# Optimization experiments

Hardware: AMD Instinct MI355X
Metric: run time of the kernel (lower is better)

## Reference

```python
import jax, jax.numpy as jnp
import numpy as np

B, L, D, HD = 8, 4096, 1024, 16
H = D // HD


def setup_inputs() -> dict:
    key = jax.random.key(0)
    ks = jax.random.split(key, 16)
    s = 0.02
    return {
        "x": jax.random.normal(ks[0], (B, L, D), dtype=jnp.float32),
        "gamma": jnp.ones((D,), jnp.float32),
        "beta": jnp.zeros((D,), jnp.float32),
        "qw": jax.random.normal(ks[1], (D, D), jnp.float32) * s,
        "qb": jnp.zeros((D,), jnp.float32),
        "kw": jax.random.normal(ks[2], (D, D), jnp.float32) * s,
        "kb": jnp.zeros((D,), jnp.float32),
        "vw": jax.random.normal(ks[3], (D, D), jnp.float32) * s,
        "vb": jnp.zeros((D,), jnp.float32),
        "ow": jax.random.normal(ks[4], (D, D), jnp.float32) * s,
        "ob": jnp.zeros((D,), jnp.float32),
        "iw": jax.random.normal(ks[5], (H, D), jnp.float32) * s,
        "ib": jnp.zeros((H,), jnp.float32),
        "fw": jax.random.normal(ks[6], (H, D), jnp.float32) * s,
        "fb": jnp.zeros((H,), jnp.float32),
    }


def _layernorm(x, gamma, beta, eps=1e-5):
    mu = jnp.mean(x, axis=-1, keepdims=True)
    var = jnp.mean(jnp.square(x - mu), axis=-1, keepdims=True)
    return (x - mu) * jax.lax.rsqrt(var + eps) * gamma + beta


def _forward(x, gamma, beta, qw, qb, kw, kb, vw, vb, ow, ob, iw, ib, fw, fb):
    b, l, d = x.shape
    h_, dh = H, HD
    xn = _layernorm(x, gamma, beta)                    # [B,L,D]
    # Projections vectorized over time (the per-step norm/proj is time-independent)
    q = (xn @ qw.T + qb).reshape(b, l, h_, dh)
    k = ((xn @ kw.T + kb) / np.sqrt(dh)).reshape(b, l, h_, dh)
    v = (xn @ vw.T + vb).reshape(b, l, h_, dh)
    i_t = xn @ iw.T + ib                               # [B,L,H]
    f_t = xn @ fw.T + fb                               # [B,L,H]

    def step(carry, inp):
        C, n, m = carry
        qt, kt, vt, it, ft = inp                       # [B,H,Dh]x3, [B,H]x2
        m_new = jnp.maximum(ft + m, it)
        f = jnp.exp(ft + m - m_new)                    # [B,H]
        i = jnp.exp(it - m_new)                        # [B,H]
        vk = jnp.einsum('bhd,bhe->bhde', vt, kt)
        C_new = f[..., None, None] * C + i[..., None, None] * vk
        n_new = f[..., None] * n + i[..., None] * kt
        Cq = jnp.einsum('bhde,bhd->bhe', C_new, qt)
        denom = jnp.maximum(jnp.abs(jnp.sum(n_new * qt, axis=-1, keepdims=True)), 1.0)
        ht = (Cq / denom).reshape(b, d)
        return (C_new, n_new, m_new), ht

    init = (jnp.zeros((b, h_, dh, dh), x.dtype),
            jnp.zeros((b, h_, dh), x.dtype),
            jnp.zeros((b, h_), x.dtype))
    xs = (jnp.swapaxes(q, 0, 1), jnp.swapaxes(k, 0, 1), jnp.swapaxes(v, 0, 1),
          jnp.swapaxes(i_t, 0, 1), jnp.swapaxes(f_t, 0, 1))
    _, hs = jax.lax.scan(step, init, xs)               # [L,B,D]
    hs = jnp.swapaxes(hs, 0, 1)                        # [B,L,D]
    out = hs @ ow.T + ob
    return x + out                                     # dropout is identity in eval


def reference(x, gamma, beta, qw, qb, kw, kb, vw, vb, ow, ob, iw, ib, fw, fb):
    return _forward(x, gamma, beta, qw, qb, kw, kb, vw, vb, ow, ob, iw, ib, fw, fb)
```

## Files before the change

### kernel.cpp

```cpp
#include <hip/hip_runtime.h>
#include <stdint.h>

#define Bq 8
#define Lq 4096
#define Dq 1024
#define Hq 64
#define Mq (Bq*Lq)
#define CH 64
#define NC (Lq/CH)
#define TC (Bq*Hq*NC)
#define RECF 288

typedef short bf16x8 __attribute__((ext_vector_type(8)));
typedef float f32x4  __attribute__((ext_vector_type(4)));

__device__ __forceinline__ float b2f(unsigned short u) {
  union { unsigned int i; float f; } v; v.i = ((unsigned int)u) << 16; return v.f;
}
__device__ __forceinline__ unsigned short f2b(float f) {
  union { float f; unsigned int i; } v; v.f = f;
  unsigned int r = v.i + 0x7fffu + ((v.i >> 16) & 1u);
  return (unsigned short)(r >> 16);
}
__device__ __forceinline__ bf16x8 pack8(float4 a, float4 b) {
  bf16x8 r;
  r[0] = (short)f2b(a.x); r[1] = (short)f2b(a.y); r[2] = (short)f2b(a.z); r[3] = (short)f2b(a.w);
  r[4] = (short)f2b(b.x); r[5] = (short)f2b(b.y); r[6] = (short)f2b(b.z); r[7] = (short)f2b(b.w);
  return r;
}

__global__ void classify_kernel(const unsigned short* __restrict__ w, unsigned int* flag) {
  __shared__ unsigned int s_nz, s_ib;
  if (threadIdx.x == 0) { s_nz = 0; s_ib = 0; }
  __syncthreads();
  unsigned int nz = 0, ib = 0;
  for (int i = threadIdx.x; i < 8192; i += 256) {
    unsigned short u = w[2 * i];
    if (u) {
      nz++;
      unsigned int e = (u >> 7) & 0xFFu;
      if (e >= 0x31u && e <= 0x9Du) ib++;
    }
  }
  atomicAdd(&s_nz, nz); atomicAdd(&s_ib, ib);
  __syncthreads();
  if (threadIdx.x == 0) *flag = (s_nz > 0 && 4u * s_ib >= 3u * s_nz) ? 1u : 0u;
}

__global__ void sentinel_kernel(unsigned short* out, int n) {
  int i = blockIdx.x * 256 + threadIdx.x;
  if (i < n) out[i] = 0x447A;
}

__global__ void ln_kernel(const void* __restrict__ xv,
                          const void* __restrict__ gv,
                          const void* __restrict__ bev,
                          unsigned short* __restrict__ xn,
                          const unsigned int* __restrict__ flagp) {
  const int isbf = (int)*flagp;
  const int row = blockIdx.x;
  const int t = threadIdx.x;
  const size_t base = (size_t)row * Dq;
  float v0, v1, v2, v3, g0, g1, g2, g3, e0, e1, e2, e3;
  if (isbf) {
    ushort4 u  = *(const ushort4*)((const unsigned short*)xv + base + t * 4);
    ushort4 g  = *(const ushort4*)((const unsigned short*)gv + t * 4);
    ushort4 be = *(const ushort4*)((const unsigned short*)bev + t * 4);
    v0 = b2f(u.x); v1 = b2f(u.y); v2 = b2f(u.z); v3 = b2f(u.w);
    g0 = b2f(g.x); g1 = b2f(g.y); g2 = b2f(g.z); g3 = b2f(g.w);
    e0 = b2f(be.x); e1 = b2f(be.y); e2 = b2f(be.z); e3 = b2f(be.w);
  } else {
    float4 u  = *(const float4*)((const float*)xv + base + t * 4);
    float4 g  = *(const float4*)((const float*)gv + t * 4);
    float4 be = *(const float4*)((const float*)bev + t * 4);
    v0 = u.x; v1 = u.y; v2 = u.z; v3 = u.w;
    g0 = g.x; g1 = g.y; g2 = g.z; g3 = g.w;
    e0 = be.x; e1 = be.y; e2 = be.z; e3 = be.w;
  }
  float s  = v0 + v1 + v2 + v3;
  float ss = v0*v0 + v1*v1 + v2*v2 + v3*v3;
#pragma unroll
  for (int off = 32; off >= 1; off >>= 1) {
    s  += __shfl_xor(s,  off, 64);
    ss += __shfl_xor(ss, off, 64);
  }
  __shared__ float sb[8];
  const int w = t >> 6, lane = t & 63;
  if (lane == 0) { sb[w] = s; sb[4 + w] = ss; }
  __syncthreads();
  s  = sb[0] + sb[1] + sb[2] + sb[3];
  ss = sb[4] + sb[5] + sb[6] + sb[7];
  const float mu   = s * (1.0f / Dq);
  const float var  = ss * (1.0f / Dq) - mu * mu;
  const float rstd = rsqrtf(var + 1e-5f);
  ushort4 o;
  o.x = f2b((v0 - mu) * rstd * g0 + e0);
  o.y = f2b((v1 - mu) * rstd * g1 + e1);
  o.z = f2b((v2 - mu) * rstd * g2 + e2);
  o.w = f2b((v3 - mu) * rstd * g3 + e3);
  *(ushort4*)(xn + base + t * 4) = o;
}

__global__ void gemm_bt(const unsigned short* __restrict__ A,
                        const void* __restrict__ Wv,
                        const void* __restrict__ biasv,
                        const void* __restrict__ residv,
                        void* __restrict__ out,
                        int N, int K, float scale, int out_mode, int out_layout,
                        const unsigned int* __restrict__ flagp) {
  __shared__ unsigned short smA[128 * 32];
  __shared__ unsigned short smB[128 * 32];
  const int isbf = (int)*flagp;
  const int tid  = threadIdx.x;
  const int w    = tid >> 6;
  const int lane = tid & 63;
  const int wm   = w >> 1;
  const int wn   = w & 1;
  const int row0 = blockIdx.x * 128;
  const int col0 = blockIdx.y * 128;

  const int c0 = tid, c1 = tid + 256;
  const int ar0 = row0 + (c0 >> 2), ak0 = (c0 & 3) * 8;
  const int ar1 = row0 + (c1 >> 2), ak1 = (c1 & 3) * 8;
  int br0 = col0 + (c0 >> 2), bk0 = (c0 & 3) * 8;
  int br1 = col0 + (c1 >> 2), bk1 = (c1 & 3) * 8;
  if (br0 >= N) br0 = N - 1;
  if (br1 >= N) br1 = N - 1;
  const size_t aro0 = (size_t)ar0 * K + ak0;
  const size_t aro1 = (size_t)ar1 * K + ak1;
  const size_t bro0 = (size_t)br0 * K + bk0;
  const size_t bro1 = (size_t)br1 * K + bk1;

  f32x4 acc[4][4];
#pragma unroll
  for (int i = 0; i < 4; ++i)
#pragma unroll
    for (int j = 0; j < 4; ++j) acc[i][j] = (f32x4){0.f, 0.f, 0.f, 0.f};

  const int mrow = lane & 15;
  const int kq8  = (lane >> 4) * 8;

  for (int k0 = 0; k0 < K; k0 += 32) {
    bf16x8 ta0 = *(const bf16x8*)(A + aro0 + k0);
    bf16x8 ta1 = *(const bf16x8*)(A + aro1 + k0);
    bf16x8 tb0, tb1;
    if (isbf) {
      const unsigned short* W = (const unsigned short*)Wv;
      tb0 = *(const bf16x8*)(W + bro0 + k0);
      tb1 = *(const bf16x8*)(W + bro1 + k0);
    } else {
      const float* W = (const float*)Wv;
      float4 w00 = *(const float4*)(W + bro0 + k0);
      float4 w01 = *(const float4*)(W + bro0 + k0 + 4);
      float4 w10 = *(const float4*)(W + bro1 + k0);
      float4 w11 = *(const float4*)(W + bro1 + k0 + 4);
      tb0 = pack8(w00, w01);
      tb1 = pack8(w10, w11);
    }
    __syncthreads();
    *(bf16x8*)(smA + c0 * 8) = ta0;
    *(bf16x8*)(smA + c1 * 8) = ta1;
    *(bf16x8*)(smB + c0 * 8) = tb0;
    *(bf16x8*)(smB + c1 * 8) = tb1;
    __syncthreads();
    bf16x8 a[4], bb[4];
#pragma unroll
    for (int mt = 0; mt < 4; ++mt)
      a[mt] = *(const bf16x8*)(smA + (wm * 64 + mt * 16 + mrow) * 32 + kq8);
#pragma unroll
    for (int nt = 0; nt < 4; ++nt)
      bb[nt] = *(const bf16x8*)(smB + (wn * 64 + nt * 16 + mrow) * 32 + kq8);
#pragma unroll
    for (int mt = 0; mt < 4; ++mt)
#pragma unroll
      for (int nt = 0; nt < 4; ++nt)
        acc[mt][nt] = __builtin_amdgcn_mfma_f32_16x16x32_bf16(a[mt], bb[nt], acc[mt][nt], 0, 0, 0);
  }

  const int colL = lane & 15;
  const int rq   = lane >> 4;
  const int wf32 = (out_mode == 1) || (out_mode == 2 && !isbf);
#pragma unroll
  for (int nt = 0; nt < 4; ++nt) {
    const int col = col0 + wn * 64 + nt * 16 + colL;
    if (col >= N) continue;
    const float bv = isbf ? b2f(((const unsigned short*)biasv)[col])
                          : ((const float*)biasv)[col];
#pragma unroll
    for (int mt = 0; mt < 4; ++mt) {
      const int rowb = row0 + wm * 64 + mt * 16 + rq * 4;
#pragma unroll
      for (int r = 0; r < 4; ++r) {
        const int row = rowb + r;
        size_t idx;
        if (out_layout == 1) {
          const int bb2 = row >> 12, t = row & 4095;
          idx = ((((size_t)bb2 * Hq + (col >> 4)) << 12) + t) * 16 + (col & 15);
        } else if (out_layout == 2) {
          const int bb2 = row >> 12, t = row & 4095;
          idx = (((size_t)bb2 * Hq + col) << 12) + t;
        } else {
          idx = (size_t)row * N + col;
        }
        float val = (acc[mt][nt][r] + bv) * scale;
        if (residv) {
          const size_t ridx = (size_t)row * N + col;
          val += isbf ? b2f(((const unsigned short*)residv)[ridx])
                      : ((const float*)residv)[ridx];
        }
        if (wf32) ((float*)out)[idx] = val;
        else ((unsigned short*)out)[idx] = f2b(val);
      }
    }
  }
}

__device__ __forceinline__ void deposit16(float* __restrict__ dstrow, int xw,
                                          bf16x8 lo, bf16x8 hi) {
  float t[16];
#pragma unroll
  for (int j = 0; j < 8; ++j) t[j] = b2f((unsigned short)lo[j]);
#pragma unroll
  for (int j = 0; j < 8; ++j) t[8 + j] = b2f((unsigned short)hi[j]);
#pragma unroll
  for (int qd = 0; qd < 4; ++qd) {
    *(float4*)(dstrow + ((qd << 2) ^ xw)) =
        make_float4(t[qd * 4], t[qd * 4 + 1], t[qd * 4 + 2], t[qd * 4 + 3]);
  }
}


__global__ void __launch_bounds__(64, 1)
summary_kernel(const unsigned short* __restrict__ k,
               const unsigned short* __restrict__ v,
               const float* __restrict__ itg,
               const float* __restrict__ ftg,
               float* __restrict__ sum) {
  __shared__ float sk[CH * 16], sv[CH * 16], sp[CH];
  const int bid = blockIdx.x;
  const int bh  = bid >> 6;
  const int c   = bid & 63;
  const int lane = threadIdx.x;
  const int e  = lane & 15;
  const int dg = lane >> 4;
  const int d0 = dg * 4;
  const size_t qkvb = ((size_t)bh * Lq + (size_t)c * CH) * 16;
  const size_t gb   = (size_t)bh * Lq + (size_t)c * CH;

  float fv = ftg[gb + lane];
  float iv = itg[gb + lane];
  float F = fv;
#pragma unroll
  for (int off = 1; off < 64; off <<= 1) {
    float tt = __shfl_up(F, off, 64);
    if (lane >= off) F += tt;
  }
  float wv = iv - F;
  float Ml = wv;
#pragma unroll
  for (int off = 1; off < 64; off <<= 1)
    Ml = fmaxf(Ml, __shfl_xor(Ml, off, 64));
  const float Ftot = __shfl(F, 63, 64);

  const int xw = ((lane >> 1) & 3) << 2;
  {
    const unsigned short* kp = k + qkvb + (size_t)lane * 16;
    const unsigned short* vp = v + qkvb + (size_t)lane * 16;
    bf16x8 a0 = *(const bf16x8*)kp, a1 = *(const bf16x8*)(kp + 8);
    bf16x8 b0 = *(const bf16x8*)vp, b1 = *(const bf16x8*)(vp + 8);
    deposit16(sk + lane * 16, xw, a0, a1);
    deposit16(sv + lane * 16, xw, b0, b1);
    sp[lane] = __expf(wv - Ml);
  }
  float C0 = 0, C1 = 0, C2 = 0, C3 = 0;
  float g0 = 0, g1 = 0, g2 = 0, g3 = 0;
#pragma unroll 4
  for (int s = 0; s < CH; ++s) {
    const int x = ((s >> 1) & 3) << 2;
    const float* kr = sk + s * 16;
    const float* vr = sv + s * 16;
    const float p  = sp[s];
    const float ke = kr[e ^ x];
    const float4 kq = *(const float4*)(kr + (d0 ^ x));
    const float4 vq = *(const float4*)(vr + (d0 ^ x));
    const float a = p * ke;
    C0 = fmaf(a, vq.x, C0); C1 = fmaf(a, vq.y, C1);
    C2 = fmaf(a, vq.z, C2); C3 = fmaf(a, vq.w, C3);
    g0 = fmaf(p, kq.x, g0); g1 = fmaf(p, kq.y, g1);
    g2 = fmaf(p, kq.z, g2); g3 = fmaf(p, kq.w, g3);
  }
  float* rec = sum + (size_t)bid * RECF;
  *(float4*)(rec + e * 16 + d0) = make_float4(C0, C1, C2, C3);
  if (e == 0) *(float4*)(rec + 256 + d0) = make_float4(g0, g1, g2, g3);
  if (lane == 0) { rec[272] = Ml; rec[273] = Ftot; }
}

__global__ void __launch_bounds__(64, 1)
combine_kernel(float* __restrict__ sum) {
  const int bh = blockIdx.x;
  const int lane = threadIdx.x;
  float* base = sum + (size_t)bh * NC * RECF;
  float4 Sc = make_float4(0.f, 0.f, 0.f, 0.f);
  float Sn = 0.f;
  float m = 0.f;
  float4 G = *(float4*)(base + lane * 4);
  float gn = (lane < 16) ? base[256 + lane] : 0.f;
  float Ml = base[272], F = base[273];
  for (int c = 0; c < NC; ++c) {
    float* rec = base + (size_t)c * RECF;
    float4 Gn = make_float4(0.f, 0.f, 0.f, 0.f);
    float gnn = 0.f, Mln = 0.f, Fn = 0.f;
    if (c + 1 < NC) {
      float* rn = rec + RECF;
      Gn = *(float4*)(rn + lane * 4);
      if (lane < 16) gnn = rn[256 + lane];
      Mln = rn[272]; Fn = rn[273];
    }
    *(float4*)(rec + lane * 4) = Sc;
    if (lane < 16) rec[256 + lane] = Sn;
    if (lane == 0) rec[272] = m;
    const float mx = fmaxf(m, Ml);
    const float al = __expf(m - mx);
    const float be = __expf(Ml - mx);
    Sc.x = fmaf(al, Sc.x, be * G.x);
    Sc.y = fmaf(al, Sc.y, be * G.y);
    Sc.z = fmaf(al, Sc.z, be * G.z);
    Sc.w = fmaf(al, Sc.w, be * G.w);
    Sn = fmaf(al, Sn, be * gn);
    m = F + mx;
    G = Gn; gn = gnn; Ml = Mln; F = Fn;
  }
}

__global__ void __launch_bounds__(64, 1)
chunk_scan_kernel(const unsigned short* __restrict__ q,
                  const unsigned short* __restrict__ k,
                  const unsigned short* __restrict__ v,
                  const float* __restrict__ itg,
                  const float* __restrict__ ftg,
                  const float* __restrict__ sum,
                  unsigned short* __restrict__ hout) {
  __shared__ float sk[CH * 16], sq[CH * 16], sv[CH * 16], sg[2 * CH];
  const int bid = blockIdx.x;
  const int bh  = bid >> 6;
  const int c   = bid & 63;
  const int b   = bh >> 6;
  const int h   = bh & 63;
  const int lane = threadIdx.x;
  const int e  = lane & 15;
  const int dg = lane >> 4;
  const int d0 = dg * 4;
  const size_t qkvb = ((size_t)bh * Lq + (size_t)c * CH) * 16;
  const size_t gb   = (size_t)bh * Lq + (size_t)c * CH;
  const size_t ob   = (size_t)b * Lq * Dq + (size_t)h * 16 + (size_t)c * CH * Dq;

  const float* rec = sum + (size_t)bid * RECF;
  const float4 Cv = *(const float4*)(rec + e * 16 + d0);
  const float4 nv = *(const float4*)(rec + 256 + d0);
  float m = rec[272];
  float C0 = Cv.x, C1 = Cv.y, C2 = Cv.z, C3 = Cv.w;
  float n0 = nv.x, n1 = nv.y, n2 = nv.z, n3 = nv.w;

  const int xw = ((lane >> 1) & 3) << 2;
  {
    const unsigned short* kp = k + qkvb + (size_t)lane * 16;
    const unsigned short* qp = q + qkvb + (size_t)lane * 16;
    const unsigned short* vp = v + qkvb + (size_t)lane * 16;
    bf16x8 a0 = *(const bf16x8*)kp, a1 = *(const bf16x8*)(kp + 8);
    bf16x8 b0 = *(const bf16x8*)qp, b1 = *(const bf16x8*)(qp + 8);
    bf16x8 c0v = *(const bf16x8*)vp, c1v = *(const bf16x8*)(vp + 8);
    deposit16(sk + lane * 16, xw, a0, a1);
    deposit16(sq + lane * 16, xw, b0, b1);
    deposit16(sv + lane * 16, xw, c0v, c1v);
    sg[lane] = itg[gb + lane];
    sg[CH + lane] = ftg[gb + lane];
  }

#pragma unroll 4
  for (int s = 0; s < CH; ++s) {
    const int x = ((s >> 1) & 3) << 2;
    const float* kr = sk + s * 16;
    const float* qr = sq + s * 16;
    const float* vr = sv + s * 16;
    const float itc = sg[s];
    const float ftc = sg[CH + s];
    const float ke  = kr[e ^ x];
    const float4 kq4 = *(const float4*)(kr + (d0 ^ x));
    const float4 qq4 = *(const float4*)(qr + (d0 ^ x));
    const float4 vq4 = *(const float4*)(vr + (d0 ^ x));
    const float fm = ftc + m;
    const float mn = fmaxf(fm, itc);
    const float fg = __expf(fm - mn);
    const float ig = __expf(itc - mn);
    m = mn;
    const float a = ig * ke;
    C0 = fmaf(fg, C0, a * vq4.x);
    C1 = fmaf(fg, C1, a * vq4.y);
    C2 = fmaf(fg, C2, a * vq4.z);
    C3 = fmaf(fg, C3, a * vq4.w);
    n0 = fmaf(fg, n0, ig * kq4.x);
    n1 = fmaf(fg, n1, ig * kq4.y);
    n2 = fmaf(fg, n2, ig * kq4.z);
    n3 = fmaf(fg, n3, ig * kq4.w);
    float cq = fmaf(C3, qq4.w, fmaf(C2, qq4.z, fmaf(C1, qq4.y, C0 * qq4.x)));
    float dn = fmaf(n3, qq4.w, fmaf(n2, qq4.z, fmaf(n1, qq4.y, n0 * qq4.x)));
    cq += __shfl_xor(cq, 16, 64);
    cq += __shfl_xor(cq, 32, 64);
    dn += __shfl_xor(dn, 16, 64);
    dn += __shfl_xor(dn, 32, 64);
    const float denom = fmaxf(fabsf(dn), 1.0f);
    if (dg == 0) hout[ob + (size_t)s * Dq + e] = f2b(cq / denom);
  }
}

__global__ void __launch_bounds__(64, 1)
scan_kernel(const unsigned short* __restrict__ q,
            const unsigned short* __restrict__ k,
            const unsigned short* __restrict__ v,
            const float* __restrict__ itg,
            const float* __restrict__ ftg,
            unsigned short* __restrict__ hout) {
  __shared__ float sk[CH * 16], sq[CH * 16], sv[CH * 16], sg[2 * CH];
  const int bh = blockIdx.x;
  const int b  = bh >> 6;
  const int h  = bh & 63;
  const int lane = threadIdx.x;
  const int e  = lane & 15;
  const int dg = lane >> 4;
  const int d0 = dg * 4;
  const size_t qkvb = (size_t)bh * Lq * 16;
  const size_t gb   = (size_t)bh * Lq;
  const size_t ob   = (size_t)b * Lq * Dq + (size_t)h * 16;

  float C0 = 0, C1 = 0, C2 = 0, C3 = 0;
  float n0 = 0, n1 = 0, n2 = 0, n3 = 0;
  float m = 0.f;

  bf16x8 rk0, rk1, rq0, rq1, rv0, rv1;
  float rit, rft;
  {
    const unsigned short* kp = k + qkvb + (size_t)lane * 16;
    const unsigned short* qp = q + qkvb + (size_t)lane * 16;
    const unsigned short* vp = v + qkvb + (size_t)lane * 16;
    rk0 = *(const bf16x8*)kp; rk1 = *(const bf16x8*)(kp + 8);
    rq0 = *(const bf16x8*)qp; rq1 = *(const bf16x8*)(qp + 8);
    rv0 = *(const bf16x8*)vp; rv1 = *(const bf16x8*)(vp + 8);
    rit = itg[gb + lane]; rft = ftg[gb + lane];
  }

  const int xw = ((lane >> 1) & 3) << 2;
  const int NT = Lq / CH;
  for (int c = 0; c < NT; ++c) {
    deposit16(sk + lane * 16, xw, rk0, rk1);
    deposit16(sq + lane * 16, xw, rq0, rq1);
    deposit16(sv + lane * 16, xw, rv0, rv1);
    sg[lane] = rit; sg[CH + lane] = rft;
    if (c + 1 < NT) {
      const size_t off = qkvb + ((size_t)(c + 1) * CH + lane) * 16;
      const unsigned short* kp = k + off;
      const unsigned short* qp = q + off;
      const unsigned short* vp = v + off;
      rk0 = *(const bf16x8*)kp; rk1 = *(const bf16x8*)(kp + 8);
      rq0 = *(const bf16x8*)qp; rq1 = *(const bf16x8*)(qp + 8);
      rv0 = *(const bf16x8*)vp; rv1 = *(const bf16x8*)(vp + 8);
      rit = itg[gb + (size_t)(c + 1) * CH + lane];
      rft = ftg[gb + (size_t)(c + 1) * CH + lane];
    }
#pragma unroll 4
    for (int s = 0; s < CH; ++s) {
      const int x = ((s >> 1) & 3) << 2;
      const float* kr = sk + s * 16;
      const float* qr = sq + s * 16;
      const float* vr = sv + s * 16;
      const float itc = sg[s];
      const float ftc = sg[CH + s];
      const float ke  = kr[e ^ x];
      const float4 kq4 = *(const float4*)(kr + (d0 ^ x));
      const float4 qq4 = *(const float4*)(qr + (d0 ^ x));
      const float4 vq4 = *(const float4*)(vr + (d0 ^ x));
      const float fm = ftc + m;
      const float mn = fmaxf(fm, itc);
      const float fg = __expf(fm - mn);
      const float ig = __expf(itc - mn);
      m = mn;
      const float a = ig * ke;
      C0 = fmaf(fg, C0, a * vq4.x);
      C1 = fmaf(fg, C1, a * vq4.y);
      C2 = fmaf(fg, C2, a * vq4.z);
      C3 = fmaf(fg, C3, a * vq4.w);
      n0 = fmaf(fg, n0, ig * kq4.x);
      n1 = fmaf(fg, n1, ig * kq4.y);
      n2 = fmaf(fg, n2, ig * kq4.z);
      n3 = fmaf(fg, n3, ig * kq4.w);
      float cq = fmaf(C3, qq4.w, fmaf(C2, qq4.z, fmaf(C1, qq4.y, C0 * qq4.x)));
      float dn = fmaf(n3, qq4.w, fmaf(n2, qq4.z, fmaf(n1, qq4.y, n0 * qq4.x)));
      cq += __shfl_xor(cq, 16, 64);
      cq += __shfl_xor(cq, 32, 64);
      dn += __shfl_xor(dn, 16, 64);
      dn += __shfl_xor(dn, 32, 64);
      const float denom = fmaxf(fabsf(dn), 1.0f);
      if (dg == 0) hout[ob + (size_t)(c * CH + s) * Dq + e] = f2b(cq / denom);
    }
  }
}

extern "C" void kernel_launch(void* const* d_in, const int* in_sizes, int n_in,
                              void* d_out, int out_size, void* d_ws, size_t ws_size,
                              hipStream_t stream) {
  const void* x     = d_in[0];
  const void* gamma = d_in[1];
  const void* beta  = d_in[2];
  const void* qw    = d_in[3];
  const void* qbv   = d_in[4];
  const void* kw    = d_in[5];
  const void* kbv   = d_in[6];
  const void* vw    = d_in[7];
  const void* vbv   = d_in[8];
  const void* ow    = d_in[9];
  const void* obv   = d_in[10];
  const void* iw    = d_in[11];
  const void* ibv   = d_in[12];
  const void* fw    = d_in[13];
  const void* fbv   = d_in[14];

  const size_t bufBytes  = (size_t)Mq * Dq * 2;
  const size_t gateBytes = (size_t)Mq * Hq * 4;
  const size_t sumBytes  = (size_t)TC * RECF * 4;
  const size_t need_old   = 4 * bufBytes + 2 * gateBytes + 4096;
  const size_t need_chunk = need_old + sumBytes;
  if (ws_size < need_old) {
    sentinel_kernel<<<(out_size + 255) / 256, 256, 0, stream>>>((unsigned short*)d_out, out_size);
    return;
  }
  const int chunked = (ws_size >= need_chunk);

  char* ws = (char*)d_ws;
  unsigned short* xnb = (unsigned short*)ws; ws += bufBytes;
  unsigned short* qbf = (unsigned short*)ws; ws += bufBytes;
  unsigned short* kbf = (unsigned short*)ws; ws += bufBytes;
  unsigned short* vbf = (unsigned short*)ws; ws += bufBytes;
  float* itb = (float*)ws; ws += gateBytes;
  float* ftb = (float*)ws; ws += gateBytes;
  unsigned int* flagp = (unsigned int*)ws; ws += 4096;
  float* sumb = (float*)ws;
  unsigned short* hbf = xnb;

  classify_kernel<<<1, 256, 0, stream>>>((const unsigned short*)qw, flagp);
  ln_kernel<<<Mq, 256, 0, stream>>>(x, gamma, beta, xnb, flagp);
  gemm_bt<<<dim3(Mq / 128, 8), 256, 0, stream>>>(xnb, qw, qbv, nullptr, qbf, Dq, Dq, 1.0f,  0, 1, flagp);
  gemm_bt<<<dim3(Mq / 128, 8), 256, 0, stream>>>(xnb, kw, kbv, nullptr, kbf, Dq, Dq, 0.25f, 0, 1, flagp);
  gemm_bt<<<dim3(Mq / 128, 8), 256, 0, stream>>>(xnb, vw, vbv, nullptr, vbf, Dq, Dq, 1.0f,  0, 1, flagp);
  gemm_bt<<<dim3(Mq / 128, 1), 256, 0, stream>>>(xnb, iw, ibv, nullptr, itb, Hq, Dq, 1.0f,  1, 2, flagp);
  gemm_bt<<<dim3(Mq / 128, 1), 256, 0, stream>>>(xnb, fw, fbv, nullptr, ftb, Hq, Dq, 1.0f,  1, 2, flagp);
  if (chunked) {
    summary_kernel<<<TC, 64, 0, stream>>>(kbf, vbf, itb, ftb, sumb);
    combine_kernel<<<Bq * Hq, 64, 0, stream>>>(sumb);
    chunk_scan_kernel<<<TC, 64, 0, stream>>>(qbf, kbf, vbf, itb, ftb, sumb, hbf);
  } else {
    scan_kernel<<<Bq * Hq, 64, 0, stream>>>(qbf, kbf, vbf, itb, ftb, hbf);
  }
  gemm_bt<<<dim3(Mq / 128, 8), 256, 0, stream>>>(hbf, ow, obv, x, d_out, Dq, Dq, 1.0f, 2, 0, flagp);
}
```

Baseline: 1.260 ms.

## Pre-convert weights to bf16 and use direct global-to-LDS loads in projection GEMMs

Adds a weight conversion kernel that writes the Q/K/V/O weights as bf16 into workspace, and a new gemm16 kernel that streams A and W tiles straight into LDS with global_load_lds. This removes the per-tile fp32-to-bf16 conversion and register staging from the four large GEMMs. It costs four extra small launches and needs more workspace, and falls back to the old path when the workspace is too small. The LDS layout has no swizzle, so bank conflicts on the fragment reads are possible.

```diff
diff --git a/kernel.cpp b/kernel.cpp
--- a/kernel.cpp
+++ b/kernel.cpp
@@ -27,6 +27,12 @@
   r[0] = (short)f2b(a.x); r[1] = (short)f2b(a.y); r[2] = (short)f2b(a.z); r[3] = (short)f2b(a.w);
   r[4] = (short)f2b(b.x); r[5] = (short)f2b(b.y); r[6] = (short)f2b(b.z); r[7] = (short)f2b(b.w);
   return r;
+}
+
+__device__ __forceinline__ void gload_lds16(const unsigned short* g, unsigned short* l) {
+  __builtin_amdgcn_global_load_lds(
+      (const __attribute__((address_space(1))) unsigned int*)g,
+      (__attribute__((address_space(3))) unsigned int*)l, 16, 0, 0);
 }
 
 __global__ void classify_kernel(const unsigned short* __restrict__ w, unsigned int* flag) {
@@ -50,6 +56,20 @@
 __global__ void sentinel_kernel(unsigned short* out, int n) {
   int i = blockIdx.x * 256 + threadIdx.x;
   if (i < n) out[i] = 0x447A;
+}
+
+__global__ void wconv_kernel(const void* __restrict__ wv, unsigned short* __restrict__ o,
+                             const unsigned int* __restrict__ flagp) {
+  const int isbf = (int)*flagp;
+  const size_t i = ((size_t)blockIdx.x * 256 + threadIdx.x) * 8;
+  if (isbf) {
+    *(bf16x8*)(o + i) = *(const bf16x8*)((const unsigned short*)wv + i);
+  } else {
+    const float* wf = (const float*)wv;
+    float4 a = *(const float4*)(wf + i);
+    float4 b = *(const float4*)(wf + i + 4);
+    *(bf16x8*)(o + i) = pack8(a, b);
+  }
 }
 
 __global__ void ln_kernel(const void* __restrict__ xv,
@@ -101,6 +121,48 @@
   *(ushort4*)(xn + base + t * 4) = o;
 }
 
+__device__ __forceinline__ void gemm_epilogue(
+    f32x4 acc[4][4], int row0, int col0, int wm, int wn, int lane,
+    const void* biasv, const void* residv, void* out,
+    int N, float scale, int out_mode, int out_layout, int isbf) {
+  const int colL = lane & 15;
+  const int rq   = lane >> 4;
+  const int wf32 = (out_mode == 1) || (out_mode == 2 && !isbf);
+#pragma unroll
+  for (int nt = 0; nt < 4; ++nt) {
+    const int col = col0 + wn * 64 + nt * 16 + colL;
+    if (col >= N) continue;
+    const float bv = isbf ? b2f(((const unsigned short*)biasv)[col])
+                          : ((const float*)biasv)[col];
+#pragma unroll
+    for (int mt = 0; mt < 4; ++mt) {
+      const int rowb = row0 + wm * 64 + mt * 16 + rq * 4;
+#pragma unroll
+      for (int r = 0; r < 4; ++r) {
+        const int row = rowb + r;
+        size_t idx;
+        if (out_layout == 1) {
+          const int bb2 = row >> 12, t = row & 4095;
+          idx = ((((size_t)bb2 * Hq + (col >> 4)) << 12) + t) * 16 + (col & 15);
+        } else if (out_layout == 2) {
+          const int bb2 = row >> 12, t = row & 4095;
+          idx = (((size_t)bb2 * Hq + col) << 12) + t;
+        } else {
+          idx = (size_t)row * N + col;
+        }
+        float val = (acc[mt][nt][r] + bv) * scale;
+        if (residv) {
+          const size_t ridx = (size_t)row * N + col;
+          val += isbf ? b2f(((const unsigned short*)residv)[ridx])
+                      : ((const float*)residv)[ridx];
+        }
+        if (wf32) ((float*)out)[idx] = val;
+        else ((unsigned short*)out)[idx] = f2b(val);
+      }
+    }
+  }
+}
+
 __global__ void gemm_bt(const unsigned short* __restrict__ A,
                         const void* __restrict__ Wv,
                         const void* __restrict__ biasv,
@@ -176,43 +238,70 @@
       for (int nt = 0; nt < 4; ++nt)
         acc[mt][nt] = __builtin_amdgcn_mfma_f32_16x16x32_bf16(a[mt], bb[nt], acc[mt][nt], 0, 0, 0);
   }
-
-  const int colL = lane & 15;
-  const int rq   = lane >> 4;
-  const int wf32 = (out_mode == 1) || (out_mode == 2 && !isbf);
-#pragma unroll
-  for (int nt = 0; nt < 4; ++nt) {
-    const int col = col0 + wn * 64 + nt * 16 + colL;
-    if (col >= N) continue;
-    const float bv = isbf ? b2f(((const unsigned short*)biasv)[col])
-                          : ((const float*)biasv)[col];
-#pragma unroll
-    for (int mt = 0; mt < 4; ++mt) {
-      const int rowb = row0 + wm * 64 + mt * 16 + rq * 4;
-#pragma unroll
-      for (int r = 0; r < 4; ++r) {
-        const int row = rowb + r;
-        size_t idx;
-        if (out_layout == 1) {
-          const int bb2 = row >> 12, t = row & 4095;
-          idx = ((((size_t)bb2 * Hq + (col >> 4)) << 12) + t) * 16 + (col & 15);
-        } else if (out_layout == 2) {
-          const int bb2 = row >> 12, t = row & 4095;
-          idx = (((size_t)bb2 * Hq + col) << 12) + t;
-        } else {
-          idx = (size_t)row * N + col;
-        }
-        float val = (acc[mt][nt][r] + bv) * scale;
-        if (residv) {
-          const size_t ridx = (size_t)row * N + col;
-          val += isbf ? b2f(((const unsigned short*)residv)[ridx])
-                      : ((const float*)residv)[ridx];
-        }
-        if (wf32) ((float*)out)[idx] = val;
-        else ((unsigned short*)out)[idx] = f2b(val);
-      }
-    }
-  }
+  gemm_epilogue(acc, row0, col0, wm, wn, lane, biasv, residv, out,
+                N, scale, out_mode, out_layout, isbf);
+}
+
+__global__ void __launch_bounds__(256)
+gemm16(const unsigned short* __restrict__ A,
+       const unsigned short* __restrict__ W,
+       const void* __restrict__ biasv,
+       const void* __restrict__ residv,
+       void* __restrict__ out,
+       float scale, int out_mode, int out_layout,
+       const unsigned int* __restrict__ flagp) {
+  __shared__ unsigned short smA[128 * 32];
+  __shared__ unsigned short smB[128 * 32];
+  const int isbf = (int)*flagp;
+  const int tid  = threadIdx.x;
+  const int w    = tid >> 6;
+  const int lane = tid & 63;
+  const int wm   = w >> 1;
+  const int wn   = w & 1;
+  const int row0 = blockIdx.x * 128;
+  const int col0 = blockIdx.y * 128;
+
+  const int rA0 = (w * 2) * 16 + (lane >> 2);
+  const size_t aoff0 = (size_t)(row0 + rA0) * Dq + (lane & 3) * 8;
+  const size_t aoff1 = aoff0 + (size_t)16 * Dq;
+  const size_t boff0 = (size_t)(col0 + rA0) * Dq + (lane & 3) * 8;
+  const size_t boff1 = boff0 + (size_t)16 * Dq;
+  unsigned short* ldsA0 = smA + w * 1024;
+  unsigned short* ldsA1 = smA + w * 1024 + 512;
+  unsigned short* ldsB0 = smB + w * 1024;
+  unsigned short* ldsB1 = smB + w * 1024 + 512;
+
+  f32x4 acc[4][4];
+#pragma unroll
+  for (int i = 0; i < 4; ++i)
+#pragma unroll
+    for (int j = 0; j < 4; ++j) acc[i][j] = (f32x4){0.f, 0.f, 0.f, 0.f};
+
+  const int mrow = lane & 15;
+  const int kq8  = (lane >> 4) * 8;
+
+  for (int k0 = 0; k0 < Dq; k0 += 32) {
+    __syncthreads();
+    gload_lds16(A + aoff0 + k0, ldsA0);
+    gload_lds16(A + aoff1 + k0, ldsA1);
+    gload_lds16(W + boff0 + k0, ldsB0);
+    gload_lds16(W + boff1 + k0, ldsB1);
+    __syncthreads();
+    bf16x8 a[4], bb[4];
+#pragma unroll
+    for (int mt = 0; mt < 4; ++mt)
+      a[mt] = *(const bf16x8*)(smA + (wm * 64 + mt * 16 + mrow) * 32 + kq8);
+#pragma unroll
+    for (int nt = 0; nt < 4; ++nt)
+      bb[nt] = *(const bf16x8*)(smB + (wn * 64 + nt * 16 + mrow) * 32 + kq8);
+#pragma unroll
+    for (int mt = 0; mt < 4; ++mt)
+#pragma unroll
+      for (int nt = 0; nt < 4; ++nt)
+        acc[mt][nt] = __builtin_amdgcn_mfma_f32_16x16x32_bf16(a[mt], bb[nt], acc[mt][nt], 0, 0, 0);
+  }
+  gemm_epilogue(acc, row0, col0, wm, wn, lane, biasv, residv, out,
+                Dq, scale, out_mode, out_layout, isbf);
 }
 
 __device__ __forceinline__ void deposit16(float* __restrict__ dstrow, int xw,
@@ -526,13 +615,16 @@
   const size_t bufBytes  = (size_t)Mq * Dq * 2;
   const size_t gateBytes = (size_t)Mq * Hq * 4;
   const size_t sumBytes  = (size_t)TC * RECF * 4;
+  const size_t wBytes    = (size_t)Dq * Dq * 2;
   const size_t need_old   = 4 * bufBytes + 2 * gateBytes + 4096;
   const size_t need_chunk = need_old + sumBytes;
+  const size_t need_fast  = need_chunk + 4 * wBytes;
   if (ws_size < need_old) {
     sentinel_kernel<<<(out_size + 255) / 256, 256, 0, stream>>>((unsigned short*)d_out, out_size);
     return;
   }
   const int chunked = (ws_size >= need_chunk);
+  const int fast    = (ws_size >= need_fast);
 
   char* ws = (char*)d_ws;
   unsigned short* xnb = (unsigned short*)ws; ws += bufBytes;
@@ -542,14 +634,29 @@
   float* itb = (float*)ws; ws += gateBytes;
   float* ftb = (float*)ws; ws += gateBytes;
   unsigned int* flagp = (unsigned int*)ws; ws += 4096;
-  float* sumb = (float*)ws;
+  float* sumb = (float*)ws; ws += sumBytes;
+  unsigned short* wqb = (unsigned short*)ws; ws += wBytes;
+  unsigned short* wkb = (unsigned short*)ws; ws += wBytes;
+  unsigned short* wvb = (unsigned short*)ws; ws += wBytes;
+  unsigned short* wob = (unsigned short*)ws; ws += wBytes;
   unsigned short* hbf = xnb;
 
   classify_kernel<<<1, 256, 0, stream>>>((const unsigned short*)qw, flagp);
   ln_kernel<<<Mq, 256, 0, stream>>>(x, gamma, beta, xnb, flagp);
-  gemm_bt<<<dim3(Mq / 128, 8), 256, 0, stream>>>(xnb, qw, qbv, nullptr, qbf, Dq, Dq, 1.0f,  0, 1, flagp);
-  gemm_bt<<<dim3(Mq / 128, 8), 256, 0, stream>>>(xnb, kw, kbv, nullptr, kbf, Dq, Dq, 0.25f, 0, 1, flagp);
-  gemm_bt<<<dim3(Mq / 128, 8), 256, 0, stream>>>(xnb, vw, vbv, nullptr, vbf, Dq, Dq, 1.0f,  0, 1, flagp);
+  if (fast) {
+    const int wgrid = (Dq * Dq / 8) / 256;
+    wconv_kernel<<<wgrid, 256, 0, stream>>>(qw, wqb, flagp);
+    wconv_kernel<<<wgrid, 256, 0, stream>>>(kw, wkb, flagp);
+    wconv_kernel<<<wgrid, 256, 0, stream>>>(vw, wvb, flagp);
+    wconv_kernel<<<wgrid, 256, 0, stream>>>(ow, wob, flagp);
+    gemm16<<<dim3(Mq / 128, Dq / 128), 256, 0, stream>>>(xnb, wqb, qbv, nullptr, qbf, 1.0f,  0, 1, flagp);
+    gemm16<<<dim3(Mq / 128, Dq / 128), 256, 0, stream>>>(xnb, wkb, kbv, nullptr, kbf, 0.25f, 0, 1, flagp);
+    gemm16<<<dim3(Mq / 128, Dq / 128), 256, 0, stream>>>(xnb, wvb, vbv, nullptr, vbf, 1.0f,  0, 1, flagp);
+  } else {
+    gemm_bt<<<dim3(Mq / 128, 8), 256, 0, stream>>>(xnb, qw, qbv, nullptr, qbf, Dq, Dq, 1.0f,  0, 1, flagp);
+    gemm_bt<<<dim3(Mq / 128, 8), 256, 0, stream>>>(xnb, kw, kbv, nullptr, kbf, Dq, Dq, 0.25f, 0, 1, flagp);
+    gemm_bt<<<dim3(Mq / 128, 8), 256, 0, stream>>>(xnb, vw, vbv, nullptr, vbf, Dq, Dq, 1.0f,  0, 1, flagp);
+  }
   gemm_bt<<<dim3(Mq / 128, 1), 256, 0, stream>>>(xnb, iw, ibv, nullptr, itb, Hq, Dq, 1.0f,  1, 2, flagp);
   gemm_bt<<<dim3(Mq / 128, 1), 256, 0, stream>>>(xnb, fw, fbv, nullptr, ftb, Hq, Dq, 1.0f,  1, 2, flagp);
   if (chunked) {
@@ -559,5 +666,9 @@
   } else {
     scan_kernel<<<Bq * Hq, 64, 0, stream>>>(qbf, kbf, vbf, itb, ftb, hbf);
   }
-  gemm_bt<<<dim3(Mq / 128, 8), 256, 0, stream>>>(hbf, ow, obv, x, d_out, Dq, Dq, 1.0f, 2, 0, flagp);
-}
+  if (fast) {
+    gemm16<<<dim3(Mq / 128, Dq / 128), 256, 0, stream>>>(hbf, wob, obv, x, d_out, 1.0f, 2, 0, flagp);
+  } else {
+    gemm_bt<<<dim3(Mq / 128, 8), 256, 0, stream>>>(hbf, ow, obv, x, d_out, Dq, Dq, 1.0f, 2, 0, flagp);
+  }
+}
```

Measured after the change: 1.215 ms. 3.6% less time.
